# Kernel optimization log

Measured on AMD Instinct MI355X. Metric: run time of the kernel, lower is better.

## Reference

```python
import jax, jax.numpy as jnp
import numpy as np

EPS = 1e-5

def inorm(x):
    # instance norm over time (last) axis; torch.std is unbiased (ddof=1)
    m = jnp.mean(x, axis=-1, keepdims=True)
    s = jnp.sqrt(jnp.var(x, axis=-1, ddof=1, keepdims=True))
    return (x - m) / (s + EPS)

def tinorm(x):
    # time-wise instance norm: normalize over channel axis (dim=1)
    m = jnp.mean(x, axis=1, keepdims=True)
    s = jnp.sqrt(jnp.var(x, axis=1, ddof=1, keepdims=True))
    return (x - m) / (s + EPS)

def adaptive_norm(src, trg, wq, wk, wv, norm_fn):
    # src, trg: [B,C,T]; wq/wk/wv: [out,in] as in nn.Linear
    temp = src.shape[1] ** 0.5
    q = jnp.einsum('bct,oc->bto', norm_fn(src), wq)        # [B,Ts,C]
    k = jnp.einsum('bct,oc->bto', norm_fn(trg), wk)        # [B,Tt,C]
    v = jnp.einsum('bct,oc->bto', trg, wv)                 # [B,Tt,C]
    attn = jax.nn.softmax(jnp.einsum('bsc,btc->bst', q / temp, k), axis=-1)
    mean = jnp.einsum('bst,btc->bsc', attn, v)             # attn-weighted mean
    var = jax.nn.relu(jnp.einsum('bst,btc->bsc', attn, v * v) - mean * mean)
    mean_c = jnp.mean(mean, axis=1)[:, :, None]            # [B,C,1]
    std_c = jnp.sqrt(jnp.mean(var, axis=1))[:, :, None]    # [B,C,1]
    return std_c * inorm(src) + mean_c

def sap(x, w, b):
    # self-attention pooling over axis 1; x: [B,N,C], w: [C], b: [1]
    a = jax.nn.softmax(jnp.einsum('bnc,c->bn', x, w) + b, axis=-1)
    return jnp.einsum('bnc,bn->bc', x, a)

def setup_inputs():
    key = jax.random.key(0)
    ks = jax.random.split(key, 24)
    B, C, Ts, Tt, S = 4, 512, 2048, 2048, 2048
    sc = 1.0 / np.sqrt(C).astype(np.float32)
    return {
        'src': jax.random.normal(ks[0], (B, C, Ts), jnp.float32),
        'trg': jax.random.normal(ks[1], (B, C, Tt), jnp.float32),
        'means': jax.random.normal(ks[2], (B, S, C), jnp.float32),
        'stds': jax.random.uniform(ks[3], (B, S, C), jnp.float32),
        'wq_t': jax.random.normal(ks[4], (C, C), jnp.float32) * sc,
        'wk_t': jax.random.normal(ks[5], (C, C), jnp.float32) * sc,
        'wv_t': jax.random.normal(ks[6], (C, C), jnp.float32) * sc,
        'wq_c': jax.random.normal(ks[7], (C, C), jnp.float32) * sc,
        'wk_c': jax.random.normal(ks[8], (C, C), jnp.float32) * sc,
        'wv_c': jax.random.normal(ks[9], (C, C), jnp.float32) * sc,
        'conv1_w': jax.random.normal(ks[10], (C, 2 * C), jnp.float32) * sc,
        'conv1_b': jax.random.normal(ks[11], (C,), jnp.float32) * 0.02,
        'conv2_w': jax.random.normal(ks[12], (C, C, 3), jnp.float32) * sc,
        'bn_g': jax.random.uniform(ks[13], (C,), jnp.float32, 0.5, 1.5),
        'bn_b': jax.random.normal(ks[14], (C,), jnp.float32) * 0.05,
        'bn_m': jax.random.normal(ks[15], (C,), jnp.float32) * 0.1,
        'bn_v': jax.random.uniform(ks[16], (C,), jnp.float32, 0.5, 1.5),
        'msap_w': jax.random.normal(ks[17], (C,), jnp.float32) * sc,
        'msap_b': jax.random.normal(ks[18], (1,), jnp.float32) * 0.02,
        'ssap_w': jax.random.normal(ks[19], (C,), jnp.float32) * sc,
        'ssap_b': jax.random.normal(ks[20], (1,), jnp.float32) * 0.02,
    }

def reference(src, trg, means, stds, wq_t, wk_t, wv_t, wq_c, wk_c, wv_c,
              conv1_w, conv1_b, conv2_w, bn_g, bn_b, bn_m, bn_v,
              msap_w, msap_b, ssap_w, ssap_b):
    src1 = adaptive_norm(src, trg, wq_t, wk_t, wv_t, tinorm)   # TAN
    src2 = adaptive_norm(src, trg, wq_c, wk_c, wv_c, inorm)    # CAN
    x = jnp.concatenate([src1, src2], axis=1)                  # [B,2C,T]
    # conv1: kernel_size=1 -> pointwise GEMM
    x = jnp.einsum('bct,oc->bot', x, conv1_w) + conv1_b[None, :, None]
    # conv2: Conv1d(k=3, pad=1, bias=False) + BatchNorm1d(eval) + ReLU
    x = jax.lax.conv_general_dilated(x, conv2_w, (1,), 'SAME',
                                     dimension_numbers=('NCH', 'OIH', 'NCH'))
    x = (x - bn_m[None, :, None]) * jax.lax.rsqrt(bn_v[None, :, None] + EPS)
    x = x * bn_g[None, :, None] + bn_b[None, :, None]
    x = jax.nn.relu(x)
    # GLAN
    mean = sap(means, msap_w, msap_b)[:, :, None]              # [B,C,1]
    std = sap(stds, ssap_w, ssap_b)[:, :, None]                # [B,C,1]
    return inorm(x) * std + mean
```

## Files before the change

kernel.cpp:

```cpp
#include <hip/hip_runtime.h>
#include <cstdint>
#include <cstddef>

#define B_ 4
#define C_ 512
#define T_ 2048
#define S_ 2048
#define EPSF 1e-5f

typedef __bf16 bf16;
typedef __attribute__((ext_vector_type(8))) __bf16 bf16x8;
typedef __attribute__((ext_vector_type(4))) float f32x4;

__device__ __forceinline__ bf16 f2b(float f){ return (bf16)f; }
__device__ __forceinline__ float b2f(bf16 h){ return (float)h; }

__device__ __forceinline__ void gl_lds16(const void* g, void* l){
  __builtin_amdgcn_global_load_lds((__attribute__((address_space(1))) void*)(g),
                                   (__attribute__((address_space(3))) void*)(l), 16, 0, 0);
}

__device__ __forceinline__ float wave_sum(float v){
#pragma unroll
  for (int o = 32; o; o >>= 1) v += __shfl_xor(v, o, 64);
  return v;
}
__device__ __forceinline__ float wave_max(float v){
#pragma unroll
  for (int o = 32; o; o >>= 1) v = fmaxf(v, __shfl_xor(v, o, 64));
  return v;
}

template<int EPI, int TNW, int GX = 0, int GY = 0, int NZ = 0>
__global__ void __launch_bounds__(256) gemm_nt(
    const bf16* __restrict__ A, const bf16* __restrict__ Bm, void* __restrict__ Cout,
    int K, int lda, int ldb, int ldc,
    long long sA, long long sB, long long sC, long long sCb,
    int zdivA, int zmodB, float scale,
    const float* __restrict__ rs, const float* __restrict__ rsh,
    const float* __restrict__ cbias,
    float* __restrict__ osum, float* __restrict__ osum2, long long sRs,
    float* __restrict__ ocol)
{
  constexpr int TN = TNW*32;
  __shared__ alignas(16) bf16 lA[128*64];
  __shared__ alignas(16) bf16 lB[TN*64];
  __shared__ float redcs[EPI == 3 ? 32*68 : 1];
  const int tid = threadIdx.x;

  int bxv, byv, z;
  if constexpr (GX > 0) {
    const int bid = blockIdx.x;
    const int xcd = bid & 7, slot = bid >> 3;
    constexpr int NB  = GX*GY;
    constexpr int ZPX = (NZ >= 8) ? NZ/8 : 1;
    constexpr int XPZ = (NZ >= 8) ? 1 : 8/NZ;
    z = (xcd / XPZ) * ZPX + ((ZPX > 1) ? slot / NB : 0);
    const int inner = (ZPX > 1) ? (slot % NB)
                                : (slot + (xcd % XPZ) * (NB / XPZ));
    bxv = inner % GX; byv = inner / GX;
  } else {
    bxv = blockIdx.x; byv = blockIdx.y; z = blockIdx.z;
  }

  const bf16* Ab = A + (long long)(z / zdivA) * sA;
  const bf16* Bb = Bm + (long long)(z % zmodB) * sB;
  const int m0 = byv*128, n0 = bxv*TN;
  const int lane = tid & 63, wvi = tid >> 6;
  const int wm = wvi >> 1, wn = wvi & 1;

  f32x4 acc[4][TNW] = {};

  const int lrow = tid >> 3;
  const int lcol = ((tid ^ lrow) & 7) * 8;
  const bf16* pa = Ab + (long long)(m0 + lrow)*lda + lcol;
  const bf16* pb = Bb + (long long)(n0 + lrow)*ldb + lcol;
  char* sa = (char*)lA + tid*16;
  char* sb = (char*)lB + tid*16;

  const int csg = tid >> 3, csph = tid & 7;
  float linv4[4];
  if (EPI == 3) {
#pragma unroll
    for (int rr = 0; rr < 4; ++rr)
      linv4[rr] = 1.f / rs[(long long)z*sRs + (m0 + csg*4 + rr)];
  }

  for (int k0 = 0; k0 < K; k0 += 64) {
#pragma unroll
    for (int it = 0; it < 4; ++it)
      gl_lds16(pa + (long long)it*32*lda + k0, sa + it*4096);
#pragma unroll
    for (int it = 0; it < TNW; ++it)
      gl_lds16(pb + (long long)it*32*ldb + k0, sb + it*4096);
    __syncthreads();
#pragma unroll
    for (int ks = 0; ks < 2; ++ks) {
      const int kq = ks*4 + (lane >> 4);
      bf16x8 af[4], bfr[TNW];
#pragma unroll
      for (int mt = 0; mt < 4; ++mt) {
        int r = wm*64 + mt*16 + (lane & 15);
        af[mt] = *(const bf16x8*)&lA[r*64 + ((kq ^ (r & 7))*8)];
      }
#pragma unroll
      for (int nt = 0; nt < TNW; ++nt) {
        int r = wn*(TNW*16) + nt*16 + (lane & 15);
        bfr[nt] = *(const bf16x8*)&lB[r*64 + ((kq ^ (r & 7))*8)];
      }
#pragma unroll
      for (int mt = 0; mt < 4; ++mt)
#pragma unroll
        for (int nt = 0; nt < TNW; ++nt)
          acc[mt][nt] = __builtin_amdgcn_mfma_f32_16x16x32_bf16(af[mt], bfr[nt], acc[mt][nt], 0, 0, 0);
    }
    bool own = false;
    if (EPI == 3) {
      own = ((k0 >> 6) & 3) == bxv;
      if (own) {
        float part[8] = {0.f,0.f,0.f,0.f,0.f,0.f,0.f,0.f};
#pragma unroll
        for (int rr = 0; rr < 4; ++rr) {
          const int r = csg*4 + rr;
          bf16x8 v = *(const bf16x8*)&lA[r*64 + ((csph ^ (r & 7))*8)];
          const float li = linv4[rr];
#pragma unroll
          for (int j = 0; j < 8; ++j) part[j] += b2f(v[j]) * li;
        }
#pragma unroll
        for (int j = 0; j < 8; ++j) redcs[csg*68 + csph*8 + j] = part[j];
      }
    }
    __syncthreads();
    if (EPI == 3) {
      if (own && tid < 64) {
        float s = 0.f;
#pragma unroll
        for (int g2 = 0; g2 < 32; ++g2) s += redcs[g2*68 + tid];
        atomicAdd(&ocol[(long long)z*lda + k0 + tid], s);
      }
    }
  }

  if (EPI == 3) {
    float* red1 = (float*)lA;
    float* red2 = red1 + 4*TNW*16;
    const int cr = (lane >> 4)*4;
    float linv[4][4];
#pragma unroll
    for (int mt = 0; mt < 4; ++mt)
#pragma unroll
      for (int i = 0; i < 4; ++i)
        linv[mt][i] = 1.f / rs[(long long)z*sRs + (m0 + wm*64 + mt*16 + cr + i)];
    float s1[TNW], s2[TNW];
#pragma unroll
    for (int nt = 0; nt < TNW; ++nt) {
      s1[nt] = 0.f; s2[nt] = 0.f;
#pragma unroll
      for (int mt = 0; mt < 4; ++mt)
#pragma unroll
        for (int i = 0; i < 4; ++i) {
          float v = acc[mt][nt][i] * linv[mt][i];
          s1[nt] += v; s2[nt] += v*v;
        }
      s1[nt] += __shfl_xor(s1[nt], 16, 64);
      s1[nt] += __shfl_xor(s1[nt], 32, 64);
      s2[nt] += __shfl_xor(s2[nt], 16, 64);
      s2[nt] += __shfl_xor(s2[nt], 32, 64);
    }
    __syncthreads();
    if (lane < 16) {
#pragma unroll
      for (int nt = 0; nt < TNW; ++nt) {
        red1[(wvi*TNW + nt)*16 + lane] = s1[nt];
        red2[(wvi*TNW + nt)*16 + lane] = s2[nt];
      }
    }
    __syncthreads();
    if (tid < 2*TN) {
      const int which = tid >= TN;
      const int col = tid - which*TN;
      const int wn2 = col / (TNW*16), rem = col % (TNW*16);
      const float* rr = which ? red2 : red1;
      float v = rr[wn2*(TNW*16) + rem] + rr[(2+wn2)*(TNW*16) + rem];
      float* dst = which ? osum2 : osum;
      atomicAdd(&dst[sCb*z + n0 + col], v);
    }
    return;
  }

  const int cr = (lane >> 4)*4, cc = lane & 15;
#pragma unroll
  for (int mt = 0; mt < 4; ++mt) {
#pragma unroll
    for (int i = 0; i < 4; ++i) {
      const int mm = m0 + wm*64 + mt*16 + cr + i;
      float rsum = 0.f, rsum2 = 0.f;
#pragma unroll
      for (int nt = 0; nt < TNW; ++nt) {
        const int nn = n0 + wn*(TNW*16) + nt*16 + cc;
        float v = acc[mt][nt][i];
        const long long co = sC*z + (long long)mm*ldc + nn;
        if (EPI == 0) {
          v *= scale;
          if (cbias) v += cbias[sCb*z + nn];
          ((bf16*)Cout)[co] = f2b(v);
        } else if (EPI == 2) {
          v = fmaxf(v*rs[mm] + rsh[mm], 0.f);
          ((float*)Cout)[co] = v;
          rsum += v; rsum2 += v*v;
        } else if (EPI == 4) {
          v = __expf(v);
          ((bf16*)Cout)[co] = f2b(v);
          rsum += v;
        } else if (EPI == 5) {
          v = v*rs[(long long)z*sRs + mm] + rsh[(long long)z*sRs + mm]*cbias[sCb*z + nn];
          ((bf16*)Cout)[co] = f2b(v);
        }
      }
      if (EPI == 2 || EPI == 4) {
        rsum += __shfl_xor(rsum, 1, 64); rsum += __shfl_xor(rsum, 2, 64);
        rsum += __shfl_xor(rsum, 4, 64); rsum += __shfl_xor(rsum, 8, 64);
        if (EPI == 2) {
          rsum2 += __shfl_xor(rsum2, 1, 64); rsum2 += __shfl_xor(rsum2, 2, 64);
          rsum2 += __shfl_xor(rsum2, 4, 64); rsum2 += __shfl_xor(rsum2, 8, 64);
        }
        if (cc == 0) {
          atomicAdd(&osum[(long long)z*sRs + mm], rsum);
          if (EPI == 2) atomicAdd(&osum2[(long long)z*sRs + mm], rsum2);
        }
      }
    }
  }
}

__global__ void __launch_bounds__(512, 2) qk_exp_k(
    const bf16* __restrict__ QK, bf16* __restrict__ P, float* __restrict__ lsum)
{
  __shared__ alignas(16) char lds[135168];
  const int tid = threadIdx.x;
  const int bid = blockIdx.x;
  const int xcd = bid & 7, slot = bid >> 3;
  const int z  = (xcd >> 1) + ((slot >> 5) << 2);
  const int t  = (slot & 31) + ((xcd & 1) << 5);
  const int by = t >> 3, bx = t & 7;
  const int ph = z >> 2, b = z & 3;
  const bf16* Qb = QK + (long long)(b*2 + ph) * (2048LL*512);
  const bf16* Kb = QK + (long long)(8 + b*2 + ph) * (2048LL*512);
  const int m0 = by * 256, n0 = bx * 256;
  const int lane = tid & 63, wvi = tid >> 6;
  const int wm = wvi >> 2, wn = wvi & 3;
  const int l15 = lane & 15, lq = lane >> 4;
  const int swz = l15 & 7;

  f32x4 acc[8][4] = {};

  const int lr = tid >> 3;
  const int lc = ((tid ^ lr) & 7) * 8;
  const bf16* pa = Qb + (long long)(m0 + lr)*512 + lc;
  const bf16* pb = Kb + (long long)(n0 + lr)*512 + lc;

  auto STAGE = [&](int bb, int kt) {
    char* da = (char*)lds + bb*65536 + tid*16;
    const bf16* ga = pa + kt*64;
    const bf16* gb = pb + kt*64;
#pragma unroll
    for (int it = 0; it < 4; ++it) gl_lds16(ga + it*64*512, da + it*8192);
#pragma unroll
    for (int it = 0; it < 4; ++it) gl_lds16(gb + it*64*512, da + 32768 + it*8192);
  };

  STAGE(0, 0);
  for (int kt = 0; kt < 8; ++kt) {
    const int cur = kt & 1;
    if (kt < 7) {
      STAGE(cur ^ 1, kt + 1);
      asm volatile("s_waitcnt vmcnt(8)" ::: "memory");
    } else {
      asm volatile("s_waitcnt vmcnt(0)" ::: "memory");
    }
    __builtin_amdgcn_s_barrier();

    const bf16* lA = (const bf16*)(lds + cur*65536);
    const bf16* lB = lA + 16384;

    bf16x8 af[4], bfr[4];
#pragma unroll
    for (int half = 0; half < 4; ++half) {
      const int ks = half >> 1, mg = (half & 1) * 4;
      const int kq = ks*4 + lq;
      const int ko = (kq ^ swz) * 8;
      if ((half & 1) == 0) {
#pragma unroll
        for (int nt = 0; nt < 4; ++nt)
          bfr[nt] = *(const bf16x8*)&lB[(wn*64 + nt*16 + l15)*64 + ko];
      }
#pragma unroll
      for (int mt = 0; mt < 4; ++mt)
        af[mt] = *(const bf16x8*)&lA[(wm*128 + (mg + mt)*16 + l15)*64 + ko];
      __builtin_amdgcn_s_barrier();
      __builtin_amdgcn_s_setprio(1);
#pragma unroll
      for (int mt = 0; mt < 4; ++mt)
#pragma unroll
        for (int nt = 0; nt < 4; ++nt)
          acc[mg + mt][nt] = __builtin_amdgcn_mfma_f32_16x16x32_bf16(
              af[mt], bfr[nt], acc[mg + mt][nt], 0, 0, 0);
      __builtin_amdgcn_s_setprio(0);
      __builtin_amdgcn_s_barrier();
    }
  }

  constexpr int LDC = 264;
  bf16* lC = (bf16*)lds;
  const long long zT = (long long)z * 2048;
  float* lrw = lsum + zT;
  const int cr = lq * 4;
#pragma unroll
  for (int mt = 0; mt < 8; ++mt) {
#pragma unroll
    for (int i = 0; i < 4; ++i) {
      const int mmL = wm*128 + mt*16 + cr + i;
      float rsum = 0.f;
#pragma unroll
      for (int nt = 0; nt < 4; ++nt) {
        const int nnL = wn*64 + nt*16 + l15;
        float v = __expf(acc[mt][nt][i]);
        lC[mmL*LDC + nnL] = f2b(v);
        rsum += v;
      }
      rsum += __shfl_xor(rsum, 1, 64); rsum += __shfl_xor(rsum, 2, 64);
      rsum += __shfl_xor(rsum, 4, 64); rsum += __shfl_xor(rsum, 8, 64);
      if (l15 == 0) atomicAdd(&lrw[m0 + mmL], rsum);
    }
  }
  __syncthreads();
  bf16* Cb = P + zT * 2048;
#pragma unroll
  for (int j = 0; j < 16; ++j) {
    const int flat = j*512 + tid;
    const int r = flat >> 5, c16 = flat & 31;
    const f32x4 v = *(const f32x4*)&lC[r*LDC + c16*8];
    *(f32x4*)&Cb[(long long)(m0 + r)*2048 + n0 + c16*8] = v;
  }
}

__global__ void __launch_bounds__(256) transform_stats_k(
    const float* __restrict__ src, const float* __restrict__ trg,
    bf16* __restrict__ XT, float* __restrict__ rsum, float* __restrict__ rsum2,
    float* __restrict__ csum, float* __restrict__ csum2)
{
  __shared__ float tile[64][33];
  __shared__ float rp1[64][4], rp2[64][4];
  __shared__ float cp1[32][8], cp2[32][8];
  const int z = blockIdx.z, t0 = blockIdx.x*32, c0 = blockIdx.y*64;
  const int is_t = z >= B_, b = z & (B_-1);
  const float* X = is_t ? trg : src;
  const int tid = threadIdx.x;
  const int tx = tid & 31, cy = tid >> 5;
#pragma unroll
  for (int it = 0; it < 8; ++it) {
    const int cl = cy + it*8;
    tile[cl][tx] = X[((long long)b*C_ + c0 + cl)*T_ + t0 + tx];
  }
  __syncthreads();
  const int l32 = tid & 31, tq = tid >> 5;
#pragma unroll
  for (int r = 0; r < 4; ++r) {
    const int tl = r*8 + tq;
    bf16 b0 = f2b(tile[2*l32][tl]), b1 = f2b(tile[2*l32+1][tl]);
    unsigned short u0, u1;
    __builtin_memcpy(&u0, &b0, 2); __builtin_memcpy(&u1, &b1, 2);
    const unsigned int pk = (unsigned int)u0 | ((unsigned int)u1 << 16);
    *(unsigned int*)&XT[((long long)z*T_ + t0 + tl)*C_ + c0 + 2*l32] = pk;
  }
  {
    const int cl = tid >> 2, g = tid & 3;
    float s1 = 0.f, s2 = 0.f;
#pragma unroll
    for (int k = 0; k < 8; ++k){ float v = tile[cl][g + 4*k]; s1 += v; s2 += v*v; }
    rp1[cl][g] = s1; rp2[cl][g] = s2;
  }
  {
    const int tl = tid >> 3, g = tid & 7;
    float s1 = 0.f, s2 = 0.f;
#pragma unroll
    for (int k = 0; k < 8; ++k){ float v = tile[g + 8*k][tl]; s1 += v; s2 += v*v; }
    cp1[tl][g] = s1; cp2[tl][g] = s2;
  }
  __syncthreads();
  if (tid < 64) {
    float s1 = rp1[tid][0]+rp1[tid][1]+rp1[tid][2]+rp1[tid][3];
    float s2 = rp2[tid][0]+rp2[tid][1]+rp2[tid][2]+rp2[tid][3];
    atomicAdd(&rsum[z*C_ + c0 + tid], s1);
    atomicAdd(&rsum2[z*C_ + c0 + tid], s2);
  } else if (tid < 96) {
    const int tl = tid - 64;
    float s1 = 0.f, s2 = 0.f;
#pragma unroll
    for (int g = 0; g < 8; ++g){ s1 += cp1[tl][g]; s2 += cp2[tl][g]; }
    atomicAdd(&csum[z*T_ + t0 + tl], s1);
    atomicAdd(&csum2[z*T_ + t0 + tl], s2);
  }
}

__global__ void __launch_bounds__(256) statfin_k(
    const float* __restrict__ rsum, const float* __restrict__ rsum2,
    const float* __restrict__ csum, const float* __restrict__ csum2,
    float* __restrict__ inm, float* __restrict__ ins,
    float* __restrict__ tnm, float* __restrict__ tns)
{
  const int i = blockIdx.x*256 + threadIdx.x;
  if (i < 2*B_*C_) {
    const float s1 = rsum[i], s2 = rsum2[i];
    const float m = s1 * (1.f/T_);
    const float var = (s2 - s1*m) * (1.f/(T_-1));
    inm[i] = m; ins[i] = sqrtf(fmaxf(var, 0.f));
  } else {
    const int j = i - 2*B_*C_;
    const float s1 = csum[j], s2 = csum2[j];
    const float m = s1 * (1.f/C_);
    const float var = (s2 - s1*m) * (1.f/(C_-1));
    tnm[j] = m; tns[j] = sqrtf(fmaxf(var, 0.f));
  }
}

__global__ void __launch_bounds__(256) foldqk_k(
    const float* __restrict__ wq_c, const float* __restrict__ wq_t,
    const float* __restrict__ wk_c, const float* __restrict__ wk_t,
    const float* __restrict__ inm, const float* __restrict__ ins,
    bf16* __restrict__ W, float* __restrict__ cb)
{
  __shared__ float r1[4];
  const int o = blockIdx.x, z = blockIdx.y;
  const int side = z >> 3, b = (z >> 1) & 3, ph = z & 1;
  const float* w = side ? (ph ? wk_t : wk_c) : (ph ? wq_t : wq_c);
  const float sc = side ? 1.f : 0.044194173824159216f;
  const int ofs = (side*B_ + b)*C_;
  float acc = 0.f;
  for (int c = threadIdx.x; c < C_; c += 256) {
    float wv = w[o*C_ + c] * sc;
    float out, contrib;
    if (ph == 0) {
      float ri = 1.f / (ins[ofs + c] + EPSF);
      out = wv * ri;
      contrib = -out * inm[ofs + c];
    } else {
      out = wv;
      contrib = wv;
    }
    W[((long long)z*C_ + o)*C_ + c] = f2b(out);
    acc += contrib;
  }
  acc = wave_sum(acc);
  const int lane = threadIdx.x & 63, wq = threadIdx.x >> 6;
  if (!lane) r1[wq] = acc;
  __syncthreads();
  if (threadIdx.x == 0) cb[z*C_ + o] = r1[0]+r1[1]+r1[2]+r1[3];
}

__global__ void __launch_bounds__(256) rsfill_k(
    const float* __restrict__ tnm, const float* __restrict__ tns,
    float* __restrict__ rsq, float* __restrict__ rshq)
{
  const int z = blockIdx.y, t = blockIdx.x*256 + threadIdx.x;
  const int side = z >> 3, b = (z >> 1) & 3, ph = z & 1;
  float rv, rh;
  if (ph == 0) { rv = 1.f; rh = 1.f; }
  else {
    const int ofs = (side*B_ + b)*T_;
    float r = 1.f / (tns[ofs + t] + EPSF);
    rv = r; rh = -tnm[ofs + t] * r;
  }
  rsq[z*T_ + t] = rv; rshq[z*T_ + t] = rh;
}

__global__ void __launch_bounds__(256) softmax_row_k(const float* __restrict__ X, float* __restrict__ O)
{
  __shared__ float red[4];
  const long long row = blockIdx.x;
  const float* x = X + row*T_ + threadIdx.x*8;
  float v[8];
  f32x4 a0 = *(const f32x4*)x;
  f32x4 a1 = *(const f32x4*)(x + 4);
#pragma unroll
  for (int j = 0; j < 4; ++j){ v[j] = a0[j]; v[4+j] = a1[j]; }
  float m = -3.4e38f;
#pragma unroll
  for (int j = 0; j < 8; ++j) m = fmaxf(m, v[j]);
  m = wave_max(m);
  const int lane = threadIdx.x & 63, w = threadIdx.x >> 6;
  if (!lane) red[w] = m;
  __syncthreads();
  m = fmaxf(fmaxf(red[0], red[1]), fmaxf(red[2], red[3]));
  __syncthreads();
  float s = 0.f;
#pragma unroll
  for (int j = 0; j < 8; ++j){ v[j] = __expf(v[j] - m); s += v[j]; }
  s = wave_sum(s);
  if (!lane) red[w] = s;
  __syncthreads();
  s = red[0]+red[1]+red[2]+red[3];
  const float inv = 1.f/s;
  float* o = O + row*T_ + threadIdx.x*8;
#pragma unroll
  for (int j = 0; j < 8; ++j) o[j] = v[j]*inv;
}

__global__ void __launch_bounds__(256) vv_fin_k(const float* __restrict__ cs,
    const bf16* __restrict__ VT, const float* __restrict__ msum,
    const float* __restrict__ m2sum, float* __restrict__ meanc, float* __restrict__ stdc)
{
  __shared__ float r1[4];
  const int c = blockIdx.x, z = blockIdx.y;
  const bf16* vr = VT + ((long long)z*C_ + c)*T_;
  const float* w = cs + z*T_;
  float a = 0.f;
  for (int t = threadIdx.x; t < T_; t += 256){ float v = b2f(vr[t]); a += w[t]*v*v; }
  a = wave_sum(a);
  const int lane = threadIdx.x & 63, wq = threadIdx.x >> 6;
  if (!lane) r1[wq] = a;
  __syncthreads();
  if (threadIdx.x == 0){
    a = r1[0]+r1[1]+r1[2]+r1[3];
    const int idx = z*C_ + c;
    meanc[idx] = msum[idx] * (1.f/S_);
    float var = (a - m2sum[idx]) * (1.f/S_);
    stdc[idx] = sqrtf(fmaxf(var, 0.f));
  }
}

__global__ void __launch_bounds__(256) weff_k(const float* __restrict__ w1,
    const float* __restrict__ b1, const float* __restrict__ sdt, const float* __restrict__ sdc,
    const float* __restrict__ mct, const float* __restrict__ mcc,
    const float* __restrict__ inm, const float* __restrict__ ins,
    bf16* __restrict__ Weff, float* __restrict__ beff)
{
  __shared__ float r1[4];
  const int o = blockIdx.x, b = blockIdx.y;
  const int ofs = b*C_;
  float accb = 0.f;
  for (int c = threadIdx.x; c < C_; c += 256) {
    float wa = w1[o*2*C_ + c], wb = w1[o*2*C_ + C_ + c];
    float s = wa*sdt[b*C_+c] + wb*sdc[b*C_+c];
    float w2 = s / (ins[ofs + c] + EPSF);
    Weff[((long long)(b*C_ + o))*C_ + c] = f2b(w2);
    accb += wa*mct[b*C_+c] + wb*mcc[b*C_+c] - w2*inm[ofs + c];
  }
  accb = wave_sum(accb);
  const int lane = threadIdx.x & 63, w = threadIdx.x >> 6;
  if (!lane) r1[w] = accb;
  __syncthreads();
  if (threadIdx.x == 0) beff[b*C_ + o] = b1[o] + r1[0]+r1[1]+r1[2]+r1[3];
}

__global__ void __launch_bounds__(256) w2r_k(const float* __restrict__ w2,
    const float* __restrict__ g, const float* __restrict__ be,
    const float* __restrict__ mu, const float* __restrict__ va,
    bf16* __restrict__ W2r, float* __restrict__ bnsc, float* __restrict__ bnsh)
{
  const int o = blockIdx.x;
  for (int c = threadIdx.x; c < C_; c += 256)
#pragma unroll
    for (int dt = 0; dt < 3; ++dt)
      W2r[(long long)o*3*C_ + dt*C_ + c] = f2b(w2[((long long)o*C_ + c)*3 + dt]);
  if (threadIdx.x == 0) {
    float s = g[o] * rsqrtf(va[o] + EPSF);
    bnsc[o] = s;
    bnsh[o] = be[o] - mu[o]*s;
  }
}

__global__ void __launch_bounds__(256) castv_k(const float* __restrict__ a0,
    const float* __restrict__ a1, bf16* __restrict__ o)
{
  const int i = blockIdx.x*256 + threadIdx.x;
  o[i] = f2b(((i >> 18) ? a1 : a0)[i & 262143]);
}

__global__ void __launch_bounds__(256) zero_pad_k(bf16* __restrict__ x1p)
{
  const int i = blockIdx.x*256 + threadIdx.x;
  const int b = i >> 10, rem = i & 1023;
  const long long row = (rem >> 9) ? (T_+1) : 0;
  const int c = rem & (C_-1);
  x1p[((long long)b*(T_+2) + row)*C_ + c] = f2b(0.f);
}

__global__ void __launch_bounds__(256) zero_f32_k(float* __restrict__ p)
{
  p[blockIdx.x*256 + threadIdx.x] = 0.f;
}

__global__ void __launch_bounds__(256) sap_logit_k(const float* __restrict__ means,
    const float* __restrict__ stds, const float* __restrict__ mw, const float* __restrict__ sw,
    const float* __restrict__ mb, const float* __restrict__ sb, float* __restrict__ out)
{
  const int n = blockIdx.x*4 + (threadIdx.x >> 6);
  const int z = blockIdx.y;
  const int sel = z >= B_, b = z & (B_-1);
  const float* x = sel ? stds : means;
  const float* w = sel ? sw : mw;
  const int lane = threadIdx.x & 63;
  const float* p = x + ((long long)b*S_ + n)*C_;
  float a = 0.f;
  for (int c = lane; c < C_; c += 64) a += p[c]*w[c];
  a = wave_sum(a);
  if (!lane) out[z*S_ + n] = a + (sel ? sb[0] : mb[0]);
}

__global__ void __launch_bounds__(256) sap_wsum_k(const float* __restrict__ means,
    const float* __restrict__ stds, const float* __restrict__ a, float* __restrict__ out)
{
  const int c = blockIdx.x*256 + threadIdx.x;
  const int z = blockIdx.z;
  const int sel = z >= B_, b = z & (B_-1);
  const float* x = sel ? stds : means;
  const long long n0 = (long long)blockIdx.y*256;
  const float* p = x + ((long long)b*S_ + n0)*C_ + c;
  const float* aw = a + z*S_ + n0;
  float acc = 0.f;
  for (int n = 0; n < 256; ++n) acc += p[(long long)n*C_] * aw[n];
  atomicAdd(&out[z*C_ + c], acc);
}

__global__ void __launch_bounds__(256) final_k(const float* __restrict__ y,
    const float* __restrict__ ysum, const float* __restrict__ y2sum,
    const float* __restrict__ sapms, float* __restrict__ out)
{
  const long long i = (long long)(blockIdx.x*256 + threadIdx.x) * 4;
  const long long r = i >> 11;
  const float s1 = ysum[r], s2 = y2sum[r];
  const float m = s1 * (1.f/T_);
  const float var = (s2 - s1*m) * (1.f/(T_-1));
  const float inv = 1.f/(sqrtf(fmaxf(var, 0.f)) + EPSF);
  const float mn = sapms[r], sd = sapms[B_*C_ + r];
  const f32x4 v = *(const f32x4*)(y + i);
  f32x4 o;
#pragma unroll
  for (int j = 0; j < 4; ++j) o[j] = (v[j] - m)*inv*sd + mn;
  *(f32x4*)(out + i) = o;
}

extern "C" void kernel_launch(void* const* d_in, const int* in_sizes, int n_in,
                              void* d_out, int out_size, void* d_ws, size_t ws_size,
                              hipStream_t stream)
{
  (void)in_sizes; (void)n_in; (void)out_size; (void)ws_size;
  const float* src    = (const float*)d_in[0];
  const float* trg    = (const float*)d_in[1];
  const float* means  = (const float*)d_in[2];
  const float* stds   = (const float*)d_in[3];
  const float* conv1w = (const float*)d_in[10];
  const float* conv1b = (const float*)d_in[11];
  const float* conv2w = (const float*)d_in[12];
  const float* bn_g   = (const float*)d_in[13];
  const float* bn_b   = (const float*)d_in[14];
  const float* bn_m   = (const float*)d_in[15];
  const float* bn_v   = (const float*)d_in[16];
  const float* msap_w = (const float*)d_in[17];
  const float* msap_b = (const float*)d_in[18];
  const float* ssap_w = (const float*)d_in[19];
  const float* ssap_b = (const float*)d_in[20];

  const long long BTC = (long long)B_*T_*C_;
  const long long TC  = (long long)T_*C_;

  char* p = (char*)d_ws;
  auto take = [&](size_t n)->char*{ char* r = p; p += (n + 255) & ~(size_t)255; return r; };

  bf16* P2  = (bf16*)take((size_t)2*B_*S_*T_*2);
  bf16* QK4 = (bf16*)take((size_t)16*TC*2);
  bf16* VT2 = (bf16*)take((size_t)2*BTC*2);
  bf16* WQeff = (bf16*)take((size_t)16*C_*C_*2);
  bf16* WVb = (bf16*)take((size_t)2*C_*C_*2);
  bf16* Weff= (bf16*)take((size_t)B_*C_*C_*2);
  bf16* W2r = (bf16*)take((size_t)C_*3*C_*2);
  bf16* x1p = (bf16*)take((size_t)B_*(T_+2)*C_*2);
  float* y  = (float*)take((size_t)B_*C_*T_*4);
  bf16* XT  = (bf16*)y;
  float* colsum = (float*)take(2*B_*T_*4);
  float* msum   = (float*)take(2*B_*C_*4);
  float* m2sum  = (float*)take(2*B_*C_*4);
  float* sapms  = (float*)take(2*B_*C_*4);
  float* lrow   = (float*)take(2*B_*S_*4);
  float* ysum   = (float*)take(B_*C_*4);
  float* y2sum  = (float*)take(B_*C_*4);
  float* rsum   = (float*)take(2*B_*C_*4);
  float* rsum2  = (float*)take(2*B_*C_*4);
  float* csum   = (float*)take(2*B_*T_*4);
  float* csum2  = (float*)take(2*B_*T_*4);
  float* tnm = (float*)take(2*B_*T_*4);
  float* tns = (float*)take(2*B_*T_*4);
  float* inm = (float*)take(2*B_*C_*4);
  float* ins = (float*)take(2*B_*C_*4);
  float* meanc = (float*)take(2*B_*C_*4);
  float* stdc  = (float*)take(2*B_*C_*4);
  float* beff  = (float*)take(B_*C_*4);
  float* bnsc  = (float*)take(C_*4);
  float* bnsh  = (float*)take(C_*4);
  float* sapl  = (float*)take(2*B_*S_*4);
  float* sapa  = (float*)take(2*B_*S_*4);
  float* cbq   = (float*)take(16*C_*4);
  float* rsq   = (float*)take(16*T_*4);
  float* rshq  = (float*)take(16*T_*4);

  dim3 blk(256);

  zero_f32_k<<<352, blk, 0, stream>>>(colsum);
  castv_k<<<2048, blk, 0, stream>>>((const float*)d_in[9], (const float*)d_in[6], WVb);
  w2r_k<<<C_, blk, 0, stream>>>(conv2w, bn_g, bn_b, bn_m, bn_v, W2r, bnsc, bnsh);
  transform_stats_k<<<dim3(T_/32, C_/64, 2*B_), blk, 0, stream>>>(src, trg, XT,
      rsum, rsum2, csum, csum2);
  statfin_k<<<80, blk, 0, stream>>>(rsum, rsum2, csum, csum2, inm, ins, tnm, tns);
  foldqk_k<<<dim3(C_, 16), blk, 0, stream>>>((const float*)d_in[7], (const float*)d_in[4],
      (const float*)d_in[8], (const float*)d_in[5], inm, ins, WQeff, cbq);
  rsfill_k<<<dim3(T_/256, 16), blk, 0, stream>>>(tnm, tns, rsq, rshq);
  zero_pad_k<<<16, blk, 0, stream>>>(x1p);

  gemm_nt<5,4,4,16,16><<<dim3(1024), blk, 0, stream>>>(XT, WQeff, QK4,
      C_, C_, C_, C_, TC, (long long)C_*C_, TC, C_,
      2, 16, 1.f, rsq, rshq, cbq, nullptr, nullptr, T_, nullptr);
  gemm_nt<0,2,32,4,8><<<dim3(1024), blk, 0, stream>>>(WVb, XT + 4*TC, VT2,
      C_, C_, C_, T_, (long long)C_*C_, TC, (long long)C_*T_, 0, 4, 4, 1.f,
      nullptr, nullptr, nullptr, nullptr, nullptr, 0, nullptr);
  qk_exp_k<<<dim3(512), dim3(512), 0, stream>>>(QK4, P2, lrow);
  gemm_nt<3,4,4,16,8><<<dim3(512), blk, 0, stream>>>(P2, VT2, nullptr,
      T_, T_, T_, 0, (long long)S_*T_, (long long)C_*T_, 0, C_, 1, 8, 1.f,
      lrow, nullptr, nullptr, msum, m2sum, S_, colsum);
  vv_fin_k<<<dim3(C_, 2*B_), blk, 0, stream>>>(colsum, VT2, msum, m2sum, meanc, stdc);

  weff_k<<<dim3(C_, B_), blk, 0, stream>>>(conv1w, conv1b,
      stdc + B_*C_, stdc, meanc + B_*C_, meanc, inm, ins, Weff, beff);
  gemm_nt<0,2,8,16,4><<<dim3(512), blk, 0, stream>>>(XT, Weff, x1p + C_,
      C_, C_, C_, C_, TC, (long long)C_*C_, (long long)(T_+2)*C_, C_,
      1, 8, 1.f, nullptr, nullptr, beff, nullptr, nullptr, 0, nullptr);
  gemm_nt<2,2,32,4,4><<<dim3(512), blk, 0, stream>>>(W2r, x1p, y,
      3*C_, 3*C_, C_, T_, 0, (long long)(T_+2)*C_, (long long)C_*T_, 0,
      1, 8, 1.f, bnsc, bnsh, nullptr, ysum, y2sum, C_, nullptr);

  sap_logit_k<<<dim3(S_/4, 2*B_), blk, 0, stream>>>(means, stds, msap_w, ssap_w,
      msap_b, ssap_b, sapl);
  softmax_row_k<<<2*B_, blk, 0, stream>>>(sapl, sapa);
  sap_wsum_k<<<dim3(C_/256, S_/256, 2*B_), blk, 0, stream>>>(means, stds, sapa, sapms);

  final_k<<<4096, blk, 0, stream>>>(y, ysum, y2sum, sapms, (float*)d_out);
}
```

Measured before the change: 400.8 us.

## Single-buffer QK exp kernel, direct stores, and move mean sum into vv_fin

The QK-exp kernel drops its double-buffered global-to-LDS pipeline and its LDS-staged output. It now uses a single 64KB LDS buffer, waits for each k-tile's loads to finish, and writes exp values straight to global memory as scattered bf16 stores. This is likely meant to cut the per-block LDS footprint, though launch bounds still allow two blocks of 512 threads per CU. In exchange it loses load/compute overlap and coalesced 16-byte stores. Separately, the PV epilogue no longer reduces the attention-weighted mean. vv_fin_k recomputes it as colsum·v alongside colsum·v², removing one set of shuffles, LDS traffic and atomics.

```diff
diff --git a/kernel.cpp b/kernel.cpp
--- a/kernel.cpp
+++ b/kernel.cpp
@@ -143,8 +143,7 @@
   }
 
   if (EPI == 3) {
-    float* red1 = (float*)lA;
-    float* red2 = red1 + 4*TNW*16;
+    float* red2 = (float*)lA;
     const int cr = (lane >> 4)*4;
     float linv[4][4];
 #pragma unroll
@@ -152,39 +151,31 @@
 #pragma unroll
       for (int i = 0; i < 4; ++i)
         linv[mt][i] = 1.f / rs[(long long)z*sRs + (m0 + wm*64 + mt*16 + cr + i)];
-    float s1[TNW], s2[TNW];
+    float s2[TNW];
 #pragma unroll
     for (int nt = 0; nt < TNW; ++nt) {
-      s1[nt] = 0.f; s2[nt] = 0.f;
+      s2[nt] = 0.f;
 #pragma unroll
       for (int mt = 0; mt < 4; ++mt)
 #pragma unroll
         for (int i = 0; i < 4; ++i) {
           float v = acc[mt][nt][i] * linv[mt][i];
-          s1[nt] += v; s2[nt] += v*v;
+          s2[nt] += v*v;
         }
-      s1[nt] += __shfl_xor(s1[nt], 16, 64);
-      s1[nt] += __shfl_xor(s1[nt], 32, 64);
       s2[nt] += __shfl_xor(s2[nt], 16, 64);
       s2[nt] += __shfl_xor(s2[nt], 32, 64);
     }
     __syncthreads();
     if (lane < 16) {
 #pragma unroll
-      for (int nt = 0; nt < TNW; ++nt) {
-        red1[(wvi*TNW + nt)*16 + lane] = s1[nt];
+      for (int nt = 0; nt < TNW; ++nt)
         red2[(wvi*TNW + nt)*16 + lane] = s2[nt];
-      }
     }
     __syncthreads();
-    if (tid < 2*TN) {
-      const int which = tid >= TN;
-      const int col = tid - which*TN;
-      const int wn2 = col / (TNW*16), rem = col % (TNW*16);
-      const float* rr = which ? red2 : red1;
-      float v = rr[wn2*(TNW*16) + rem] + rr[(2+wn2)*(TNW*16) + rem];
-      float* dst = which ? osum2 : osum;
-      atomicAdd(&dst[sCb*z + n0 + col], v);
+    if (tid < TN) {
+      const int wn2 = tid / (TNW*16), rem = tid % (TNW*16);
+      float v = red2[wn2*(TNW*16) + rem] + red2[(2+wn2)*(TNW*16) + rem];
+      atomicAdd(&osum2[sCb*z + n0 + tid], v);
     }
     return;
   }
@@ -237,7 +228,7 @@
 __global__ void __launch_bounds__(512, 2) qk_exp_k(
     const bf16* __restrict__ QK, bf16* __restrict__ P, float* __restrict__ lsum)
 {
-  __shared__ alignas(16) char lds[135168];
+  __shared__ alignas(16) char lds[65536];
   const int tid = threadIdx.x;
   const int bid = blockIdx.x;
   const int xcd = bid & 7, slot = bid >> 3;
@@ -260,28 +251,20 @@
   const bf16* pa = Qb + (long long)(m0 + lr)*512 + lc;
   const bf16* pb = Kb + (long long)(n0 + lr)*512 + lc;
 
-  auto STAGE = [&](int bb, int kt) {
-    char* da = (char*)lds + bb*65536 + tid*16;
-    const bf16* ga = pa + kt*64;
-    const bf16* gb = pb + kt*64;
-#pragma unroll
-    for (int it = 0; it < 4; ++it) gl_lds16(ga + it*64*512, da + it*8192);
-#pragma unroll
-    for (int it = 0; it < 4; ++it) gl_lds16(gb + it*64*512, da + 32768 + it*8192);
-  };
-
-  STAGE(0, 0);
   for (int kt = 0; kt < 8; ++kt) {
-    const int cur = kt & 1;
-    if (kt < 7) {
-      STAGE(cur ^ 1, kt + 1);
-      asm volatile("s_waitcnt vmcnt(8)" ::: "memory");
-    } else {
-      asm volatile("s_waitcnt vmcnt(0)" ::: "memory");
-    }
+    {
+      char* da = (char*)lds + tid*16;
+      const bf16* ga = pa + kt*64;
+      const bf16* gb = pb + kt*64;
+#pragma unroll
+      for (int it = 0; it < 4; ++it) gl_lds16(ga + it*64*512, da + it*8192);
+#pragma unroll
+      for (int it = 0; it < 4; ++it) gl_lds16(gb + it*64*512, da + 32768 + it*8192);
+    }
+    asm volatile("s_waitcnt vmcnt(0)" ::: "memory");
     __builtin_amdgcn_s_barrier();
 
-    const bf16* lA = (const bf16*)(lds + cur*65536);
+    const bf16* lA = (const bf16*)lds;
     const bf16* lB = lA + 16384;
 
     bf16x8 af[4], bfr[4];
@@ -311,37 +294,27 @@
     }
   }
 
-  constexpr int LDC = 264;
-  bf16* lC = (bf16*)lds;
   const long long zT = (long long)z * 2048;
+  bf16* Cb = P + zT * 2048;
   float* lrw = lsum + zT;
   const int cr = lq * 4;
 #pragma unroll
   for (int mt = 0; mt < 8; ++mt) {
 #pragma unroll
     for (int i = 0; i < 4; ++i) {
-      const int mmL = wm*128 + mt*16 + cr + i;
+      const int mm = m0 + wm*128 + mt*16 + cr + i;
       float rsum = 0.f;
 #pragma unroll
       for (int nt = 0; nt < 4; ++nt) {
-        const int nnL = wn*64 + nt*16 + l15;
+        const int nn = n0 + wn*64 + nt*16 + l15;
         float v = __expf(acc[mt][nt][i]);
-        lC[mmL*LDC + nnL] = f2b(v);
+        Cb[(long long)mm*2048 + nn] = f2b(v);
         rsum += v;
       }
       rsum += __shfl_xor(rsum, 1, 64); rsum += __shfl_xor(rsum, 2, 64);
       rsum += __shfl_xor(rsum, 4, 64); rsum += __shfl_xor(rsum, 8, 64);
-      if (l15 == 0) atomicAdd(&lrw[m0 + mmL], rsum);
-    }
-  }
-  __syncthreads();
-  bf16* Cb = P + zT * 2048;
-#pragma unroll
-  for (int j = 0; j < 16; ++j) {
-    const int flat = j*512 + tid;
-    const int r = flat >> 5, c16 = flat & 31;
-    const f32x4 v = *(const f32x4*)&lC[r*LDC + c16*8];
-    *(f32x4*)&Cb[(long long)(m0 + r)*2048 + n0 + c16*8] = v;
+      if (l15 == 0) atomicAdd(&lrw[mm], rsum);
+    }
   }
 }
 
@@ -508,24 +481,28 @@
 }
 
 __global__ void __launch_bounds__(256) vv_fin_k(const float* __restrict__ cs,
-    const bf16* __restrict__ VT, const float* __restrict__ msum,
+    const bf16* __restrict__ VT,
     const float* __restrict__ m2sum, float* __restrict__ meanc, float* __restrict__ stdc)
 {
-  __shared__ float r1[4];
+  __shared__ float r1[4], r2[4];
   const int c = blockIdx.x, z = blockIdx.y;
   const bf16* vr = VT + ((long long)z*C_ + c)*T_;
   const float* w = cs + z*T_;
-  float a = 0.f;
-  for (int t = threadIdx.x; t < T_; t += 256){ float v = b2f(vr[t]); a += w[t]*v*v; }
-  a = wave_sum(a);
+  float a1 = 0.f, a2 = 0.f;
+  for (int t = threadIdx.x; t < T_; t += 256){
+    float v = b2f(vr[t]); float wt = w[t];
+    a1 += wt*v; a2 += wt*v*v;
+  }
+  a1 = wave_sum(a1); a2 = wave_sum(a2);
   const int lane = threadIdx.x & 63, wq = threadIdx.x >> 6;
-  if (!lane) r1[wq] = a;
+  if (!lane){ r1[wq] = a1; r2[wq] = a2; }
   __syncthreads();
   if (threadIdx.x == 0){
-    a = r1[0]+r1[1]+r1[2]+r1[3];
+    a1 = r1[0]+r1[1]+r1[2]+r1[3];
+    a2 = r2[0]+r2[1]+r2[2]+r2[3];
     const int idx = z*C_ + c;
-    meanc[idx] = msum[idx] * (1.f/S_);
-    float var = (a - m2sum[idx]) * (1.f/S_);
+    meanc[idx] = a1 * (1.f/S_);
+    float var = (a2 - m2sum[idx]) * (1.f/S_);
     stdc[idx] = sqrtf(fmaxf(var, 0.f));
   }
 }
@@ -704,6 +681,7 @@
   float* cbq   = (float*)take(16*C_*4);
   float* rsq   = (float*)take(16*T_*4);
   float* rshq  = (float*)take(16*T_*4);
+  (void)msum;
 
   dim3 blk(256);
 
@@ -727,8 +705,8 @@
   qk_exp_k<<<dim3(512), dim3(512), 0, stream>>>(QK4, P2, lrow);
   gemm_nt<3,4,4,16,8><<<dim3(512), blk, 0, stream>>>(P2, VT2, nullptr,
       T_, T_, T_, 0, (long long)S_*T_, (long long)C_*T_, 0, C_, 1, 8, 1.f,
-      lrow, nullptr, nullptr, msum, m2sum, S_, colsum);
-  vv_fin_k<<<dim3(C_, 2*B_), blk, 0, stream>>>(colsum, VT2, msum, m2sum, meanc, stdc);
+      lrow, nullptr, nullptr, nullptr, m2sum, S_, colsum);
+  vv_fin_k<<<dim3(C_, 2*B_), blk, 0, stream>>>(colsum, VT2, m2sum, meanc, stdc);
 
   weff_k<<<dim3(C_, B_), blk, 0, stream>>>(conv1w, conv1b,
       stdc + B_*C_, stdc, meanc + B_*C_, meanc, inm, ins, Weff, beff);
```

Result: slower. 413.1 us (+3.0%).
